# Kernel optimization log

Measured on AMD Instinct MI355X. Metric: run time of the kernel, lower is better.

Reference implementation:

```python
import jax, jax.numpy as jnp
import numpy as np

VOCAB = 32000
HID = 1024
HEADS = 16
HEAD_DIM = HID // HEADS
LAYERS = 8
INTER = 4 * HID
ROPE_BASE = 100000.0
EPS = 1e-5


def setup_inputs() -> dict:
    key = jax.random.key(0)
    ks = jax.random.split(key, 12)
    s = 0.02
    inp = {
        'input_ids': jax.random.randint(ks[0], (2, 2048), 0, VOCAB),
        'embed_W': jax.random.normal(ks[1], (VOCAB, HID), jnp.float32) * s,
        'Wq': jax.random.normal(ks[2], (LAYERS, HID, HID), jnp.float32) * s,
        'Wk': jax.random.normal(ks[3], (LAYERS, HID, HID), jnp.float32) * s,
        'Wv': jax.random.normal(ks[4], (LAYERS, HID, HID), jnp.float32) * s,
        'Wo': jax.random.normal(ks[5], (LAYERS, HID, HID), jnp.float32) * s,
        'Wg': jax.random.normal(ks[6], (LAYERS, HID, INTER), jnp.float32) * s,
        'Wu': jax.random.normal(ks[7], (LAYERS, HID, INTER), jnp.float32) * s,
        'Wd': jax.random.normal(ks[8], (LAYERS, INTER, HID), jnp.float32) * s,
        'norm1_w': jnp.ones((LAYERS, HID), jnp.float32),
        'norm2_w': jnp.ones((LAYERS, HID), jnp.float32),
        'final_norm_w': jnp.ones((HID,), jnp.float32),
        'head_W': jax.random.normal(ks[9], (HID, VOCAB), jnp.float32) * s,
    }
    return inp


def rms_norm(x, w):
    return x * jax.lax.rsqrt(jnp.mean(x * x, axis=-1, keepdims=True) + EPS) * w


def rope_tables(seq_len):
    freq = 1.0 / (ROPE_BASE ** (jnp.arange(0, HEAD_DIM, 2, dtype=jnp.float32) / HEAD_DIM))
    ang = jnp.arange(seq_len, dtype=jnp.float32)[:, None] * freq  # [S, d/2]
    cos = jnp.concatenate([jnp.cos(ang), jnp.cos(ang)], axis=-1)  # [S, d]
    sin = jnp.concatenate([jnp.sin(ang), jnp.sin(ang)], axis=-1)
    return cos, sin


def rotate_half(x):
    h = x.shape[-1] // 2
    return jnp.concatenate([-x[..., h:], x[..., :h]], axis=-1)


def apply_rope(q, k, cos, sin):
    # q,k: [B,S,H,D]; cos,sin: [S,D] -> broadcast over heads via [:,None,:]
    c = cos[:, None, :]
    s = sin[:, None, :]
    return q * c + rotate_half(q) * s, k * c + rotate_half(k) * s


def attention(x, wq, wk, wv, wo, cos, sin, causal_mask):
    B, S, _ = x.shape
    q = (x @ wq).reshape(B, S, HEADS, HEAD_DIM)
    k = (x @ wk).reshape(B, S, HEADS, HEAD_DIM)
    v = (x @ wv).reshape(B, S, HEADS, HEAD_DIM)
    q, k = apply_rope(q, k, cos, sin)
    scores = jnp.einsum('bqhd,bkhd->bhqk', q, k) / np.sqrt(HEAD_DIM)
    scores = jnp.clip(scores, -1000.0, 1000.0)
    scores = jnp.where(causal_mask, jnp.finfo(scores.dtype).min, scores)
    w = jax.nn.softmax(scores.astype(jnp.float32), axis=-1).astype(q.dtype)
    w = jnp.clip(w, 0.0, 1.0)
    ctx = jnp.einsum('bhqk,bkhd->bqhd', w, v).reshape(B, S, HID)
    return ctx @ wo


def reference(input_ids, embed_W, Wq, Wk, Wv, Wo, Wg, Wu, Wd, norm1_w, norm2_w, final_norm_w, head_W):
    B, S = input_ids.shape
    h = embed_W[input_ids]  # [B,S,HID]
    cos, sin = rope_tables(S)
    causal_mask = jnp.triu(jnp.ones((S, S), bool), k=1)[None, None]
    for l in range(LAYERS):
        h = h + attention(rms_norm(h, norm1_w[l]), Wq[l], Wk[l], Wv[l], Wo[l], cos, sin, causal_mask)
        hn = rms_norm(h, norm2_w[l])
        h = h + (jax.nn.silu(hn @ Wg[l]) * (hn @ Wu[l])) @ Wd[l]
    h = rms_norm(h, final_norm_w)
    logits = h @ head_W
    return logits, h
```

## Files before the change

kernel.cpp:

```cpp
#include <hip/hip_runtime.h>

#define T_TOK 4096
#define SEQ   2048
#define HID   1024
#define NH    16
#define HD    64
#define INTER 4096
#define NLAYER 8
#define VOCAB 32000

typedef short short8 __attribute__((ext_vector_type(8)));
typedef float f32x4  __attribute__((ext_vector_type(4)));

__device__ __forceinline__ unsigned short f2bf(float f){
  unsigned int u = __builtin_bit_cast(unsigned int, f);
  u += 0x7fffu + ((u >> 16) & 1u);
  return (unsigned short)(u >> 16);
}
__device__ __forceinline__ float bf2f(unsigned short b){
  unsigned int u = ((unsigned int)b) << 16;
  return __builtin_bit_cast(float, u);
}

#define GLOAD_LDS16(gsrc, ldst) \
  __builtin_amdgcn_global_load_lds((const __attribute__((address_space(1))) void*)(gsrc), \
                                   (__attribute__((address_space(3))) void*)(ldst), 16, 0, 0)

__global__ __launch_bounds__(256) void embed_kernel(const int* __restrict__ ids,
                                                    const float* __restrict__ W,
                                                    float* __restrict__ h){
  int i = blockIdx.x * 256 + threadIdx.x;
  int t = i >> 8, c = i & 255;
  ((float4*)h)[i] = ((const float4*)(W + (size_t)ids[t] * HID))[c];
}

__global__ __launch_bounds__(256) void rope_tab_kernel(float* __restrict__ cosT,
                                                       float* __restrict__ sinT){
  int i = blockIdx.x * 256 + threadIdx.x;
  int s = i >> 5, f = i & 31;
  float inv = expf(-((2.0f * (float)f) / 64.0f) * logf(100000.0f));
  float ang = (float)s * inv;
  cosT[i] = cosf(ang);
  sinT[i] = sinf(ang);
}

__global__ __launch_bounds__(256) void rmsnorm_kernel(const float* __restrict__ h,
                                                      const float* __restrict__ w,
                                                      unsigned short* __restrict__ out,
                                                      float* hcopy){
  int t = blockIdx.x, tid = threadIdx.x;
  float4 v = ((const float4*)(h + (size_t)t * HID))[tid];
  float ss = v.x*v.x + v.y*v.y + v.z*v.z + v.w*v.w;
  #pragma unroll
  for (int m = 1; m < 64; m <<= 1) ss += __shfl_xor(ss, m);
  __shared__ float red[4];
  if ((tid & 63) == 0) red[tid >> 6] = ss;
  __syncthreads();
  float r = rsqrtf((red[0] + red[1] + red[2] + red[3]) * (1.0f / HID) + 1e-5f);
  float4 wv = ((const float4*)w)[tid];
  float nx = v.x * r * wv.x;
  float ny = v.y * r * wv.y;
  float nz = v.z * r * wv.z;
  float nw = v.w * r * wv.w;
  ushort4 o;
  o.x = f2bf(nx); o.y = f2bf(ny); o.z = f2bf(nz); o.w = f2bf(nw);
  ((ushort4*)(out + (size_t)t * HID))[tid] = o;
  if (hcopy){
    float4 hv; hv.x = nx; hv.y = ny; hv.z = nz; hv.w = nw;
    ((float4*)(hcopy + (size_t)t * HID))[tid] = hv;
  }
}

__global__ __launch_bounds__(256) void rope_kernel(unsigned short* __restrict__ q,
                                                   unsigned short* __restrict__ k,
                                                   const float* __restrict__ cosT,
                                                   const float* __restrict__ sinT){
  int i = blockIdx.x * 256 + threadIdx.x;
  int t = i >> 9, rem = i & 511;
  int hh = rem >> 5, f = rem & 31;
  int s = t & (SEQ - 1);
  float c = cosT[s * 32 + f], sn = sinT[s * 32 + f];
  size_t base = (size_t)t * HID + hh * HD + f;
  float q0 = bf2f(q[base]), q1 = bf2f(q[base + 32]);
  q[base]      = f2bf(q0 * c - q1 * sn);
  q[base + 32] = f2bf(q1 * c + q0 * sn);
  float k0 = bf2f(k[base]), k1 = bf2f(k[base + 32]);
  k[base]      = f2bf(k0 * c - k1 * sn);
  k[base + 32] = f2bf(k1 * c + k0 * sn);
}

__global__ __launch_bounds__(256) void convert_w_kernel(const float* __restrict__ W,
                                                        unsigned short* __restrict__ Wt,
                                                        int K, int N){
  __shared__ unsigned short t_lds[64][72];
  W  += (size_t)blockIdx.z * K * N;
  Wt += (size_t)blockIdx.z * K * N;
  const int n0 = blockIdx.x * 64, k0 = blockIdx.y * 64;
  const int tid = threadIdx.x;
  const int tr = tid >> 4, tc = tid & 15;
  #pragma unroll
  for (int i = 0; i < 4; ++i){
    int kk = tr + i * 16;
    float4 v = *(const float4*)(W + (size_t)(k0 + kk) * N + n0 + tc * 4);
    t_lds[tc*4+0][kk] = f2bf(v.x);
    t_lds[tc*4+1][kk] = f2bf(v.y);
    t_lds[tc*4+2][kk] = f2bf(v.z);
    t_lds[tc*4+3][kk] = f2bf(v.w);
  }
  __syncthreads();
  const int n = tid >> 2, cp = tid & 3;
  #pragma unroll
  for (int j = 0; j < 2; ++j){
    int c = cp * 2 + j;
    uint4 d = *(const uint4*)(&t_lds[n][c * 8]);
    *(uint4*)(Wt + (size_t)(n0 + n) * K + k0 + ((c ^ (n & 7)) << 3)) = d;
  }
}

__device__ __forceinline__ void gemm_core(const unsigned short* __restrict__ A,
                                          const unsigned short* __restrict__ Bt,
                                          int K, int m0, int n0,
                                          unsigned short* As, unsigned short* Bs,
                                          f32x4 (&acc)[4][4]){
  const int tid = threadIdx.x;
  const int lane = tid & 63, w = tid >> 6;
  const int l15 = lane & 15, g = lane >> 4;
  const int lr = lane >> 3;
  const int lc = lane & 7;
  const int wr = w >> 1, wc = w & 1;
  const int axor = ((lc ^ lr) << 3);

  #pragma unroll
  for (int m = 0; m < 4; ++m)
    #pragma unroll
    for (int n = 0; n < 4; ++n)
      #pragma unroll
      for (int i = 0; i < 4; ++i) acc[m][n][i] = 0.0f;

  for (int kk = 0; kk < K; kk += 64){
    __syncthreads();
    #pragma unroll
    for (int i = 0; i < 4; ++i){
      int rb = (i * 4 + w) * 8;
      GLOAD_LDS16(A  + (size_t)(m0 + rb + lr) * K + kk + axor,      As + rb * 64);
      GLOAD_LDS16(Bt + (size_t)(n0 + rb + lr) * K + kk + (lc << 3), Bs + rb * 64);
    }
    __syncthreads();
    short8 a[4][2], b[4][2];
    const int x = l15 & 7;
    #pragma unroll
    for (int m = 0; m < 4; ++m){
      int row = wr * 64 + m * 16 + l15;
      a[m][0] = *(const short8*)(As + row * 64 + ((g       ^ x) << 3));
      a[m][1] = *(const short8*)(As + row * 64 + (((4 + g) ^ x) << 3));
    }
    #pragma unroll
    for (int n = 0; n < 4; ++n){
      int row = wc * 64 + n * 16 + l15;
      b[n][0] = *(const short8*)(Bs + row * 64 + ((g       ^ x) << 3));
      b[n][1] = *(const short8*)(Bs + row * 64 + (((4 + g) ^ x) << 3));
    }
    #pragma unroll
    for (int m = 0; m < 4; ++m)
      #pragma unroll
      for (int n = 0; n < 4; ++n){
        acc[m][n] = __builtin_amdgcn_mfma_f32_16x16x32_bf16(a[m][0], b[n][0], acc[m][n], 0, 0, 0);
        acc[m][n] = __builtin_amdgcn_mfma_f32_16x16x32_bf16(a[m][1], b[n][1], acc[m][n], 0, 0, 0);
      }
  }
}

template<int MODE>
__device__ __forceinline__ void gemm_epi(const f32x4 (&acc)[4][4], void* Cout,
                                         const float* __restrict__ resid,
                                         int N, int m0, int n0, int ldt){
  const int tid = threadIdx.x;
  const int lane = tid & 63, w = tid >> 6;
  const int l15 = lane & 15, g = lane >> 4;
  const int wr = w >> 1, wc = w & 1;
  #pragma unroll
  for (int m = 0; m < 4; ++m){
    #pragma unroll
    for (int n = 0; n < 4; ++n){
      int row0 = m0 + wr * 64 + m * 16 + g * 4;
      int col  = n0 + wc * 64 + n * 16 + l15;
      #pragma unroll
      for (int i = 0; i < 4; ++i){
        float v = acc[m][n][i];
        if (MODE == 0){
          ((unsigned short*)Cout)[(size_t)(row0 + i) * N + col] = f2bf(v);
        } else if (MODE == 1){
          size_t idx = (size_t)(row0 + i) * N + col;
          ((float*)Cout)[idx] = resid[idx] + v;
        } else if (MODE == 2){
          ((unsigned short*)Cout)[(size_t)col * ldt + (row0 + i)] = f2bf(v);
        } else {
          ((float*)Cout)[(size_t)(row0 + i) * N + col] = v;
        }
      }
    }
  }
}

template<int MODE>
__global__ __launch_bounds__(256) void gemm_bf16(const unsigned short* __restrict__ A,
                                                 const unsigned short* __restrict__ Bt,
                                                 void* Cout, const float* resid,
                                                 int K, int N, int ldt){
  __shared__ unsigned short As[128 * 64];
  __shared__ unsigned short Bs[128 * 64];
  f32x4 acc[4][4];
  gemm_core(A, Bt, K, blockIdx.x * 128, blockIdx.y * 128, As, Bs, acc);
  gemm_epi<MODE>(acc, Cout, resid, N, blockIdx.x * 128, blockIdx.y * 128, ldt);
}

__global__ __launch_bounds__(256) void gemm_qkv(const unsigned short* __restrict__ A,
                                                const unsigned short* __restrict__ BtQ,
                                                const unsigned short* __restrict__ BtK,
                                                const unsigned short* __restrict__ BtV,
                                                unsigned short* qb, unsigned short* kb,
                                                unsigned short* vt){
  __shared__ unsigned short As[128 * 64];
  __shared__ unsigned short Bs[128 * 64];
  const int nb = blockIdx.y, sel = nb >> 3, n0 = (nb & 7) * 128;
  const unsigned short* Bt = (sel == 0) ? BtQ : (sel == 1) ? BtK : BtV;
  f32x4 acc[4][4];
  gemm_core(A, Bt, HID, blockIdx.x * 128, n0, As, Bs, acc);
  if (sel == 0)      gemm_epi<0>(acc, qb, nullptr, HID, blockIdx.x * 128, n0, 0);
  else if (sel == 1) gemm_epi<0>(acc, kb, nullptr, HID, blockIdx.x * 128, n0, 0);
  else               gemm_epi<2>(acc, vt, nullptr, HID, blockIdx.x * 128, n0, T_TOK);
}

__global__ __launch_bounds__(256) void gemm_gu(const unsigned short* __restrict__ A,
                                               const unsigned short* __restrict__ BtG,
                                               const unsigned short* __restrict__ BtU,
                                               unsigned short* gb, unsigned short* ub){
  __shared__ unsigned short As[128 * 64];
  __shared__ unsigned short Bs[128 * 64];
  const int nb = blockIdx.y, sel = nb >> 5, n0 = (nb & 31) * 128;
  f32x4 acc[4][4];
  gemm_core(A, sel ? BtU : BtG, HID, blockIdx.x * 128, n0, As, Bs, acc);
  gemm_epi<0>(acc, sel ? ub : gb, nullptr, INTER, blockIdx.x * 128, n0, 0);
}

__global__ __launch_bounds__(256, 2) void gemm_f32b(const unsigned short* __restrict__ A,
                                                    const float* __restrict__ Bw,
                                                    float* __restrict__ Cout,
                                                    int M, int N, int K){
  __shared__ unsigned short As[128 * 32];
  __shared__ unsigned short Bs[128 * 32];
  const int tid = threadIdx.x;
  const int lane = tid & 63, wid = tid >> 6;
  const int l15 = lane & 15, g = lane >> 4;
  const int wr = wid >> 1, wc = wid & 1;
  const int m0 = blockIdx.x * 128, n0 = blockIdx.y * 128;
  const int bcol = tid & 127, bhalf = tid >> 7;
  f32x4 acc[4][4];
  #pragma unroll
  for (int m = 0; m < 4; ++m)
    #pragma unroll
    for (int n = 0; n < 4; ++n)
      #pragma unroll
      for (int i = 0; i < 4; ++i) acc[m][n][i] = 0.0f;
  for (int kk = 0; kk < K; kk += 32){
    __syncthreads();
    #pragma unroll
    for (int cc = 0; cc < 2; ++cc){
      int c = tid + cc * 256;
      int row = c >> 2, kc = (c & 3) << 3;
      uint4 d = *(const uint4*)(A + (size_t)(m0 + row) * K + kk + kc);
      *(uint4*)(&As[row * 32 + kc]) = d;
    }
    {
      const float* bp = Bw + (size_t)(kk + bhalf * 16) * N + n0 + bcol;
      float f[16];
      #pragma unroll
      for (int j = 0; j < 16; ++j) f[j] = bp[(size_t)j * N];
      unsigned int pk[8];
      #pragma unroll
      for (int j = 0; j < 8; ++j)
        pk[j] = (unsigned int)f2bf(f[2*j]) | ((unsigned int)f2bf(f[2*j+1]) << 16);
      int sw = (bcol >> 1) & 3;
      int c0 = ((bhalf << 1)     ) ^ sw;
      int c1 = ((bhalf << 1) | 1 ) ^ sw;
      uint4 w0; w0.x = pk[0]; w0.y = pk[1]; w0.z = pk[2]; w0.w = pk[3];
      uint4 w1; w1.x = pk[4]; w1.y = pk[5]; w1.z = pk[6]; w1.w = pk[7];
      *(uint4*)(&Bs[bcol * 32 + c0 * 8]) = w0;
      *(uint4*)(&Bs[bcol * 32 + c1 * 8]) = w1;
    }
    __syncthreads();
    short8 a[4], b[4];
    #pragma unroll
    for (int m = 0; m < 4; ++m)
      a[m] = *(const short8*)(&As[(wr*64 + m*16 + l15) * 32 + g*8]);
    #pragma unroll
    for (int n = 0; n < 4; ++n){
      int col = wc*64 + n*16 + l15;
      b[n] = *(const short8*)(&Bs[col * 32 + (g ^ ((col >> 1) & 3)) * 8]);
    }
    #pragma unroll
    for (int m = 0; m < 4; ++m)
      #pragma unroll
      for (int n = 0; n < 4; ++n)
        acc[m][n] = __builtin_amdgcn_mfma_f32_16x16x32_bf16(a[m], b[n], acc[m][n], 0, 0, 0);
  }
  #pragma unroll
  for (int m = 0; m < 4; ++m)
    #pragma unroll
    for (int n = 0; n < 4; ++n){
      int row0 = m0 + wr*64 + m*16 + g*4;
      int col  = n0 + wc*64 + n*16 + l15;
      #pragma unroll
      for (int i = 0; i < 4; ++i)
        Cout[(size_t)(row0 + i) * N + col] = acc[m][n][i];
    }
}

__global__ __launch_bounds__(256) void attn_kernel(const unsigned short* __restrict__ q,
                                                   const unsigned short* __restrict__ k,
                                                   const unsigned short* __restrict__ vt,
                                                   unsigned short* __restrict__ ctx){
  const int tid = threadIdx.x;
  const int lane = tid & 63, w = tid >> 6;
  const int l15 = lane & 15, g = lane >> 4;
  const int q0 = blockIdx.x * 128 + w * 32;
  const int hh = blockIdx.y;
  const int b  = blockIdx.z;
  const int tb = b * SEQ;

  __shared__ unsigned short Ks[64][72];
  __shared__ unsigned short Vs[64][72];
  __shared__ unsigned short Ps[4][2][16][72];

  short8 qa[2][2];
  #pragma unroll
  for (int qs = 0; qs < 2; ++qs)
    #pragma unroll
    for (int kd = 0; kd < 2; ++kd)
      qa[qs][kd] = *(const short8*)(q + (size_t)(tb + q0 + qs*16 + l15) * HID + hh*HD + kd*32 + g*8);

  float m_run[2][4], l_run[2][4];
  f32x4 o_acc[2][4];
  #pragma unroll
  for (int qs = 0; qs < 2; ++qs)
    #pragma unroll
    for (int i = 0; i < 4; ++i){ m_run[qs][i] = -1e30f; l_run[qs][i] = 0.0f; }
  #pragma unroll
  for (int qs = 0; qs < 2; ++qs)
    #pragma unroll
    for (int dt = 0; dt < 4; ++dt)
      #pragma unroll
      for (int i = 0; i < 4; ++i) o_acc[qs][dt][i] = 0.0f;

  const int ntile = ((blockIdx.x * 128 + 127) >> 6) + 1;
  const int sr = tid >> 2, sc = (tid & 3) * 2;
  for (int kt = 0; kt < ntile; ++kt){
    const int kv0 = kt * 64;
    __syncthreads();
    *(uint4*)(&Ks[sr][sc*8])   = *(const uint4*)(k  + (size_t)(tb+kv0+sr)*HID + hh*HD + sc*8);
    *(uint4*)(&Ks[sr][sc*8+8]) = *(const uint4*)(k  + (size_t)(tb+kv0+sr)*HID + hh*HD + sc*8+8);
    *(uint4*)(&Vs[sr][sc*8])   = *(const uint4*)(vt + (size_t)(hh*HD+sr)*T_TOK + tb + kv0 + sc*8);
    *(uint4*)(&Vs[sr][sc*8+8]) = *(const uint4*)(vt + (size_t)(hh*HD+sr)*T_TOK + tb + kv0 + sc*8+8);
    __syncthreads();

    short8 kf[4][2];
    #pragma unroll
    for (int ct = 0; ct < 4; ++ct)
      #pragma unroll
      for (int kd = 0; kd < 2; ++kd)
        kf[ct][kd] = *(const short8*)(&Ks[ct*16 + l15][kd*32 + g*8]);

    #pragma unroll
    for (int qs = 0; qs < 2; ++qs){
      float pv[4][4];
      #pragma unroll
      for (int ct = 0; ct < 4; ++ct){
        f32x4 scv;
        #pragma unroll
        for (int i = 0; i < 4; ++i) scv[i] = 0.0f;
        scv = __builtin_amdgcn_mfma_f32_16x16x32_bf16(qa[qs][0], kf[ct][0], scv, 0, 0, 0);
        scv = __builtin_amdgcn_mfma_f32_16x16x32_bf16(qa[qs][1], kf[ct][1], scv, 0, 0, 0);
        #pragma unroll
        for (int i = 0; i < 4; ++i){
          float s = scv[i] * 0.125f;
          s = fminf(fmaxf(s, -1000.0f), 1000.0f);
          int row = q0 + qs*16 + g*4 + i;
          int col = kv0 + ct*16 + l15;
          pv[ct][i] = (col > row) ? -1e30f : s;
        }
      }
      #pragma unroll
      for (int i = 0; i < 4; ++i){
        float mx = fmaxf(fmaxf(pv[0][i], pv[1][i]), fmaxf(pv[2][i], pv[3][i]));
        #pragma unroll
        for (int msk = 1; msk < 16; msk <<= 1) mx = fmaxf(mx, __shfl_xor(mx, msk));
        float mnew = fmaxf(m_run[qs][i], mx);
        float scale = __expf(m_run[qs][i] - mnew);
        float psum = 0.0f;
        #pragma unroll
        for (int ct = 0; ct < 4; ++ct){
          float p = __expf(pv[ct][i] - mnew);
          pv[ct][i] = p; psum += p;
        }
        #pragma unroll
        for (int msk = 1; msk < 16; msk <<= 1) psum += __shfl_xor(psum, msk);
        l_run[qs][i] = l_run[qs][i] * scale + psum;
        m_run[qs][i] = mnew;
        #pragma unroll
        for (int dt = 0; dt < 4; ++dt) o_acc[qs][dt][i] *= scale;
      }
      #pragma unroll
      for (int ct = 0; ct < 4; ++ct)
        #pragma unroll
        for (int i = 0; i < 4; ++i)
          Ps[w][qs][g*4 + i][ct*16 + l15] = f2bf(pv[ct][i]);
    }
    #pragma unroll
    for (int ks = 0; ks < 2; ++ks){
      short8 vb[4];
      #pragma unroll
      for (int dt = 0; dt < 4; ++dt)
        vb[dt] = *(const short8*)(&Vs[dt*16 + l15][ks*32 + g*8]);
      #pragma unroll
      for (int qs = 0; qs < 2; ++qs){
        short8 ap = *(const short8*)(&Ps[w][qs][l15][ks*32 + g*8]);
        #pragma unroll
        for (int dt = 0; dt < 4; ++dt)
          o_acc[qs][dt] = __builtin_amdgcn_mfma_f32_16x16x32_bf16(ap, vb[dt], o_acc[qs][dt], 0, 0, 0);
      }
    }
  }
  #pragma unroll
  for (int qs = 0; qs < 2; ++qs)
    #pragma unroll
    for (int dt = 0; dt < 4; ++dt)
      #pragma unroll
      for (int i = 0; i < 4; ++i){
        float o = o_acc[qs][dt][i] / l_run[qs][i];
        ctx[(size_t)(tb + q0 + qs*16 + g*4 + i) * HID + hh*HD + dt*16 + l15] = f2bf(o);
      }
}

__global__ __launch_bounds__(256) void silu_mul_kernel(unsigned short* __restrict__ gbuf,
                                                       const unsigned short* __restrict__ ubuf){
  int i = blockIdx.x * 256 + threadIdx.x;
  ushort4 gv = ((const ushort4*)gbuf)[i];
  ushort4 uv = ((const ushort4*)ubuf)[i];
  ushort4 o;
  float x;
  x = bf2f(gv.x); o.x = f2bf((x / (1.0f + __expf(-x))) * bf2f(uv.x));
  x = bf2f(gv.y); o.y = f2bf((x / (1.0f + __expf(-x))) * bf2f(uv.y));
  x = bf2f(gv.z); o.z = f2bf((x / (1.0f + __expf(-x))) * bf2f(uv.z));
  x = bf2f(gv.w); o.w = f2bf((x / (1.0f + __expf(-x))) * bf2f(uv.w));
  ((ushort4*)gbuf)[i] = o;
}

extern "C" void kernel_launch(void* const* d_in, const int* in_sizes, int n_in,
                              void* d_out, int out_size, void* d_ws, size_t ws_size,
                              hipStream_t stream){
  const int*   ids    = (const int*)d_in[0];
  const float* embedW = (const float*)d_in[1];
  const float* Wq = (const float*)d_in[2];
  const float* Wk = (const float*)d_in[3];
  const float* Wv = (const float*)d_in[4];
  const float* Wo = (const float*)d_in[5];
  const float* Wg = (const float*)d_in[6];
  const float* Wu = (const float*)d_in[7];
  const float* Wd = (const float*)d_in[8];
  const float* n1 = (const float*)d_in[9];
  const float* n2 = (const float*)d_in[10];
  const float* nf = (const float*)d_in[11];
  const float* Wh = (const float*)d_in[12];
  float* out = (float*)d_out;

  char* scb = (char*)d_out;
  unsigned short* qb  = (unsigned short*)(scb + 0);
  unsigned short* kb  = (unsigned short*)(scb + 8388608);
  unsigned short* vtb = (unsigned short*)(scb + 16777216);
  unsigned short* ctx = (unsigned short*)(scb + 25165824);
  unsigned short* gb  = (unsigned short*)(scb + 33554432);
  unsigned short* ub  = (unsigned short*)(scb + 67108864);
  float* cosT = (float*)(scb + 100663296);
  float* sinT = (float*)(scb + 100925440);
  float* h_fallback   = (float*)(scb + 104857600);
  unsigned short* WtQ = (unsigned short*)(scb + 134217728);
  unsigned short* WtK = (unsigned short*)(scb + 150994944);
  unsigned short* WtV = (unsigned short*)(scb + 167772160);
  unsigned short* WtO = (unsigned short*)(scb + 184549376);
  unsigned short* WtG = (unsigned short*)(scb + 201326592);
  unsigned short* WtU = (unsigned short*)(scb + 268435456);
  unsigned short* WtD = (unsigned short*)(scb + 335544320);

  unsigned short* xn = (unsigned short*)d_ws;
  float* h = (ws_size >= 25165824u) ? (float*)((char*)d_ws + 8388608) : h_fallback;
  unsigned short* WhT = (ws_size >= 90701824u)
                      ? (unsigned short*)((char*)d_ws + 25165824) : nullptr;

  convert_w_kernel<<<dim3(16, 16, 8), 256, 0, stream>>>(Wq, WtQ, HID, HID);
  convert_w_kernel<<<dim3(16, 16, 8), 256, 0, stream>>>(Wk, WtK, HID, HID);
  convert_w_kernel<<<dim3(16, 16, 8), 256, 0, stream>>>(Wv, WtV, HID, HID);
  convert_w_kernel<<<dim3(16, 16, 8), 256, 0, stream>>>(Wo, WtO, HID, HID);
  convert_w_kernel<<<dim3(64, 16, 8), 256, 0, stream>>>(Wg, WtG, HID, INTER);
  convert_w_kernel<<<dim3(64, 16, 8), 256, 0, stream>>>(Wu, WtU, HID, INTER);
  convert_w_kernel<<<dim3(16, 64, 8), 256, 0, stream>>>(Wd, WtD, INTER, HID);
  if (WhT)
    convert_w_kernel<<<dim3(500, 16, 1), 256, 0, stream>>>(Wh, WhT, HID, VOCAB);

  embed_kernel<<<4096, 256, 0, stream>>>(ids, embedW, h);
  rope_tab_kernel<<<256, 256, 0, stream>>>(cosT, sinT);

  for (int l = 0; l < NLAYER; ++l){
    rmsnorm_kernel<<<4096, 256, 0, stream>>>(h, n1 + l*HID, xn, nullptr);
    gemm_qkv<<<dim3(32, 24), 256, 0, stream>>>(xn, WtQ + (size_t)l*HID*HID,
                                               WtK + (size_t)l*HID*HID,
                                               WtV + (size_t)l*HID*HID, qb, kb, vtb);
    rope_kernel<<<8192, 256, 0, stream>>>(qb, kb, cosT, sinT);
    attn_kernel<<<dim3(16, 16, 2), 256, 0, stream>>>(qb, kb, vtb, ctx);
    gemm_bf16<1><<<dim3(32, 8), 256, 0, stream>>>(ctx, WtO + (size_t)l*HID*HID,
                                                  h, h, HID, HID, 0);
    rmsnorm_kernel<<<4096, 256, 0, stream>>>(h, n2 + l*HID, xn, nullptr);
    gemm_gu<<<dim3(32, 64), 256, 0, stream>>>(xn, WtG + (size_t)l*HID*INTER,
                                              WtU + (size_t)l*HID*INTER, gb, ub);
    silu_mul_kernel<<<16384, 256, 0, stream>>>(gb, ub);
    gemm_bf16<1><<<dim3(32, 8), 256, 0, stream>>>(gb, WtD + (size_t)l*HID*INTER,
                                                  h, h, INTER, HID, 0);
  }

  rmsnorm_kernel<<<4096, 256, 0, stream>>>(h, nf, xn, out + 131072000);
  if (WhT)
    gemm_bf16<3><<<dim3(32, 250), 256, 0, stream>>>(xn, WhT, out, nullptr, HID, VOCAB, 0);
  else
    gemm_f32b<<<dim3(32, 250), 256, 0, stream>>>(xn, Wh, out, T_TOK, VOCAB, HID);
}
```

Measured before the change: 3.834 ms.

## Rework GEMM K-tiling and flash attention tiling with causal skip and lazy rescale

The GEMM core drops from a 64-wide to a 32-wide K step, removes the XOR swizzle in both the weight transpose and the LDS reads, and halves LDS use per block. The f32 epilogue now uses nontemporal stores. Attention moves to 128-key tiles, launches the heaviest query blocks first, skips fully masked column tiles on the diagonal, and only rescales the running max when it grows by more than 8. This aims for better occupancy and less wasted work on masked tiles, but the unswizzled LDS layout risks bank conflicts and the shorter K step doubles the barriers per GEMM.

```diff
diff --git a/kernel.cpp b/kernel.cpp
--- a/kernel.cpp
+++ b/kernel.cpp
@@ -113,7 +113,7 @@
   for (int j = 0; j < 2; ++j){
     int c = cp * 2 + j;
     uint4 d = *(const uint4*)(&t_lds[n][c * 8]);
-    *(uint4*)(Wt + (size_t)(n0 + n) * K + k0 + ((c ^ (n & 7)) << 3)) = d;
+    *(uint4*)(Wt + (size_t)(n0 + n) * K + k0 + c * 8) = d;
   }
 }
 
@@ -125,10 +125,9 @@
   const int tid = threadIdx.x;
   const int lane = tid & 63, w = tid >> 6;
   const int l15 = lane & 15, g = lane >> 4;
-  const int lr = lane >> 3;
-  const int lc = lane & 7;
   const int wr = w >> 1, wc = w & 1;
-  const int axor = ((lc ^ lr) << 3);
+  const int srow = lane >> 2;
+  const int soff = (lane & 3) << 3;
 
   #pragma unroll
   for (int m = 0; m < 4; ++m)
@@ -137,36 +136,25 @@
       #pragma unroll
       for (int i = 0; i < 4; ++i) acc[m][n][i] = 0.0f;
 
-  for (int kk = 0; kk < K; kk += 64){
+  for (int kk = 0; kk < K; kk += 32){
     __syncthreads();
-    #pragma unroll
-    for (int i = 0; i < 4; ++i){
-      int rb = (i * 4 + w) * 8;
-      GLOAD_LDS16(A  + (size_t)(m0 + rb + lr) * K + kk + axor,      As + rb * 64);
-      GLOAD_LDS16(Bt + (size_t)(n0 + rb + lr) * K + kk + (lc << 3), Bs + rb * 64);
-    }
+    GLOAD_LDS16(A  + (size_t)(m0 +      w*16 + srow) * K + kk + soff, As + (w*16) * 32);
+    GLOAD_LDS16(A  + (size_t)(m0 + 64 + w*16 + srow) * K + kk + soff, As + (64 + w*16) * 32);
+    GLOAD_LDS16(Bt + (size_t)(n0 +      w*16 + srow) * K + kk + soff, Bs + (w*16) * 32);
+    GLOAD_LDS16(Bt + (size_t)(n0 + 64 + w*16 + srow) * K + kk + soff, Bs + (64 + w*16) * 32);
     __syncthreads();
-    short8 a[4][2], b[4][2];
-    const int x = l15 & 7;
-    #pragma unroll
-    for (int m = 0; m < 4; ++m){
-      int row = wr * 64 + m * 16 + l15;
-      a[m][0] = *(const short8*)(As + row * 64 + ((g       ^ x) << 3));
-      a[m][1] = *(const short8*)(As + row * 64 + (((4 + g) ^ x) << 3));
-    }
-    #pragma unroll
-    for (int n = 0; n < 4; ++n){
-      int row = wc * 64 + n * 16 + l15;
-      b[n][0] = *(const short8*)(Bs + row * 64 + ((g       ^ x) << 3));
-      b[n][1] = *(const short8*)(Bs + row * 64 + (((4 + g) ^ x) << 3));
-    }
+    short8 a[4], b[4];
     #pragma unroll
     for (int m = 0; m < 4; ++m)
-      #pragma unroll
-      for (int n = 0; n < 4; ++n){
-        acc[m][n] = __builtin_amdgcn_mfma_f32_16x16x32_bf16(a[m][0], b[n][0], acc[m][n], 0, 0, 0);
-        acc[m][n] = __builtin_amdgcn_mfma_f32_16x16x32_bf16(a[m][1], b[n][1], acc[m][n], 0, 0, 0);
-      }
+      a[m] = *(const short8*)(As + (wr*64 + m*16 + l15) * 32 + g*8);
+    #pragma unroll
+    for (int n = 0; n < 4; ++n)
+      b[n] = *(const short8*)(Bs + (wc*64 + n*16 + l15) * 32 + g*8);
+    #pragma unroll
+    for (int m = 0; m < 4; ++m)
+      #pragma unroll
+      for (int n = 0; n < 4; ++n)
+        acc[m][n] = __builtin_amdgcn_mfma_f32_16x16x32_bf16(a[m], b[n], acc[m][n], 0, 0, 0);
   }
 }
 
@@ -195,7 +183,7 @@
         } else if (MODE == 2){
           ((unsigned short*)Cout)[(size_t)col * ldt + (row0 + i)] = f2bf(v);
         } else {
-          ((float*)Cout)[(size_t)(row0 + i) * N + col] = v;
+          __builtin_nontemporal_store(v, &((float*)Cout)[(size_t)(row0 + i) * N + col]);
         }
       }
     }
@@ -207,8 +195,8 @@
                                                  const unsigned short* __restrict__ Bt,
                                                  void* Cout, const float* resid,
                                                  int K, int N, int ldt){
-  __shared__ unsigned short As[128 * 64];
-  __shared__ unsigned short Bs[128 * 64];
+  __shared__ unsigned short As[128 * 32];
+  __shared__ unsigned short Bs[128 * 32];
   f32x4 acc[4][4];
   gemm_core(A, Bt, K, blockIdx.x * 128, blockIdx.y * 128, As, Bs, acc);
   gemm_epi<MODE>(acc, Cout, resid, N, blockIdx.x * 128, blockIdx.y * 128, ldt);
@@ -220,8 +208,8 @@
                                                 const unsigned short* __restrict__ BtV,
                                                 unsigned short* qb, unsigned short* kb,
                                                 unsigned short* vt){
-  __shared__ unsigned short As[128 * 64];
-  __shared__ unsigned short Bs[128 * 64];
+  __shared__ unsigned short As[128 * 32];
+  __shared__ unsigned short Bs[128 * 32];
   const int nb = blockIdx.y, sel = nb >> 3, n0 = (nb & 7) * 128;
   const unsigned short* Bt = (sel == 0) ? BtQ : (sel == 1) ? BtK : BtV;
   f32x4 acc[4][4];
@@ -235,8 +223,8 @@
                                                const unsigned short* __restrict__ BtG,
                                                const unsigned short* __restrict__ BtU,
                                                unsigned short* gb, unsigned short* ub){
-  __shared__ unsigned short As[128 * 64];
-  __shared__ unsigned short Bs[128 * 64];
+  __shared__ unsigned short As[128 * 32];
+  __shared__ unsigned short Bs[128 * 32];
   const int nb = blockIdx.y, sel = nb >> 5, n0 = (nb & 31) * 128;
   f32x4 acc[4][4];
   gemm_core(A, sel ? BtU : BtG, HID, blockIdx.x * 128, n0, As, Bs, acc);
@@ -323,14 +311,14 @@
   const int tid = threadIdx.x;
   const int lane = tid & 63, w = tid >> 6;
   const int l15 = lane & 15, g = lane >> 4;
-  const int q0 = blockIdx.x * 128 + w * 32;
+  const int bx = (int)gridDim.x - 1 - (int)blockIdx.x;
+  const int q0 = bx * 128 + w * 32;
   const int hh = blockIdx.y;
-  const int b  = blockIdx.z;
-  const int tb = b * SEQ;
-
-  __shared__ unsigned short Ks[64][72];
-  __shared__ unsigned short Vs[64][72];
-  __shared__ unsigned short Ps[4][2][16][72];
+  const int tb = blockIdx.z * SEQ;
+
+  __shared__ unsigned short Ks[128][72];
+  __shared__ unsigned short Vs[64][136];
+  __shared__ unsigned short Ps[4][16][136];
 
   short8 qa[2][2];
   #pragma unroll
@@ -352,81 +340,97 @@
       #pragma unroll
       for (int i = 0; i < 4; ++i) o_acc[qs][dt][i] = 0.0f;
 
-  const int ntile = ((blockIdx.x * 128 + 127) >> 6) + 1;
-  const int sr = tid >> 2, sc = (tid & 3) * 2;
-  for (int kt = 0; kt < ntile; ++kt){
-    const int kv0 = kt * 64;
+  const int krow = tid >> 1, khf = (tid & 1) * 32;
+  const int vrow = tid >> 2, vq  = (tid & 3) * 32;
+
+  for (int kt = 0; kt <= bx; ++kt){
+    const int kv0 = kt * 128;
     __syncthreads();
-    *(uint4*)(&Ks[sr][sc*8])   = *(const uint4*)(k  + (size_t)(tb+kv0+sr)*HID + hh*HD + sc*8);
-    *(uint4*)(&Ks[sr][sc*8+8]) = *(const uint4*)(k  + (size_t)(tb+kv0+sr)*HID + hh*HD + sc*8+8);
-    *(uint4*)(&Vs[sr][sc*8])   = *(const uint4*)(vt + (size_t)(hh*HD+sr)*T_TOK + tb + kv0 + sc*8);
-    *(uint4*)(&Vs[sr][sc*8+8]) = *(const uint4*)(vt + (size_t)(hh*HD+sr)*T_TOK + tb + kv0 + sc*8+8);
+    {
+      const unsigned short* kp = k + (size_t)(tb + kv0 + krow) * HID + hh*HD + khf;
+      #pragma unroll
+      for (int j = 0; j < 4; ++j)
+        *(uint4*)(&Ks[krow][khf + j*8]) = *(const uint4*)(kp + j*8);
+      const unsigned short* vp = vt + (size_t)(hh*HD + vrow) * T_TOK + tb + kv0 + vq;
+      #pragma unroll
+      for (int j = 0; j < 4; ++j)
+        *(uint4*)(&Vs[vrow][vq + j*8]) = *(const uint4*)(vp + j*8);
+    }
     __syncthreads();
-
-    short8 kf[4][2];
-    #pragma unroll
-    for (int ct = 0; ct < 4; ++ct)
-      #pragma unroll
-      for (int kd = 0; kd < 2; ++kd)
-        kf[ct][kd] = *(const short8*)(&Ks[ct*16 + l15][kd*32 + g*8]);
+    const int nct = (kt < bx) ? 8 : (2 * w + 2);
+    const int nks = nct >> 1;
 
     #pragma unroll
     for (int qs = 0; qs < 2; ++qs){
-      float pv[4][4];
-      #pragma unroll
-      for (int ct = 0; ct < 4; ++ct){
-        f32x4 scv;
-        #pragma unroll
-        for (int i = 0; i < 4; ++i) scv[i] = 0.0f;
-        scv = __builtin_amdgcn_mfma_f32_16x16x32_bf16(qa[qs][0], kf[ct][0], scv, 0, 0, 0);
-        scv = __builtin_amdgcn_mfma_f32_16x16x32_bf16(qa[qs][1], kf[ct][1], scv, 0, 0, 0);
-        #pragma unroll
-        for (int i = 0; i < 4; ++i){
-          float s = scv[i] * 0.125f;
-          s = fminf(fmaxf(s, -1000.0f), 1000.0f);
-          int row = q0 + qs*16 + g*4 + i;
-          int col = kv0 + ct*16 + l15;
-          pv[ct][i] = (col > row) ? -1e30f : s;
+      float pv[8][4];
+      #pragma unroll
+      for (int ct = 0; ct < 8; ++ct){
+        if (ct < nct){
+          f32x4 scv;
+          #pragma unroll
+          for (int i = 0; i < 4; ++i) scv[i] = 0.0f;
+          scv = __builtin_amdgcn_mfma_f32_16x16x32_bf16(qa[qs][0],
+                  *(const short8*)(&Ks[ct*16 + l15][g*8]), scv, 0, 0, 0);
+          scv = __builtin_amdgcn_mfma_f32_16x16x32_bf16(qa[qs][1],
+                  *(const short8*)(&Ks[ct*16 + l15][32 + g*8]), scv, 0, 0, 0);
+          #pragma unroll
+          for (int i = 0; i < 4; ++i){
+            float s = scv[i] * 0.125f;
+            s = fminf(fmaxf(s, -1000.0f), 1000.0f);
+            int row = q0 + qs*16 + g*4 + i;
+            int col = kv0 + ct*16 + l15;
+            pv[ct][i] = (col > row) ? -1e30f : s;
+          }
+        } else {
+          #pragma unroll
+          for (int i = 0; i < 4; ++i) pv[ct][i] = -1e30f;
         }
       }
       #pragma unroll
       for (int i = 0; i < 4; ++i){
-        float mx = fmaxf(fmaxf(pv[0][i], pv[1][i]), fmaxf(pv[2][i], pv[3][i]));
+        float mx = pv[0][i];
+        #pragma unroll
+        for (int ct = 1; ct < 8; ++ct) mx = fmaxf(mx, pv[ct][i]);
         #pragma unroll
         for (int msk = 1; msk < 16; msk <<= 1) mx = fmaxf(mx, __shfl_xor(mx, msk));
-        float mnew = fmaxf(m_run[qs][i], mx);
-        float scale = __expf(m_run[qs][i] - mnew);
+        if (!__all(mx <= m_run[qs][i] + 8.0f)){
+          float mnew = fmaxf(m_run[qs][i], mx);
+          float scale = __expf(m_run[qs][i] - mnew);
+          m_run[qs][i] = mnew;
+          l_run[qs][i] *= scale;
+          #pragma unroll
+          for (int dt = 0; dt < 4; ++dt) o_acc[qs][dt][i] *= scale;
+        }
         float psum = 0.0f;
         #pragma unroll
-        for (int ct = 0; ct < 4; ++ct){
-          float p = __expf(pv[ct][i] - mnew);
-          pv[ct][i] = p; psum += p;
+        for (int ct = 0; ct < 8; ++ct){
+          if (ct < nct){
+            float p = __expf(pv[ct][i] - m_run[qs][i]);
+            pv[ct][i] = p; psum += p;
+          } else pv[ct][i] = 0.0f;
         }
         #pragma unroll
         for (int msk = 1; msk < 16; msk <<= 1) psum += __shfl_xor(psum, msk);
-        l_run[qs][i] = l_run[qs][i] * scale + psum;
-        m_run[qs][i] = mnew;
-        #pragma unroll
-        for (int dt = 0; dt < 4; ++dt) o_acc[qs][dt][i] *= scale;
+        l_run[qs][i] += psum;
       }
       #pragma unroll
-      for (int ct = 0; ct < 4; ++ct)
-        #pragma unroll
-        for (int i = 0; i < 4; ++i)
-          Ps[w][qs][g*4 + i][ct*16 + l15] = f2bf(pv[ct][i]);
-    }
-    #pragma unroll
-    for (int ks = 0; ks < 2; ++ks){
-      short8 vb[4];
-      #pragma unroll
-      for (int dt = 0; dt < 4; ++dt)
-        vb[dt] = *(const short8*)(&Vs[dt*16 + l15][ks*32 + g*8]);
-      #pragma unroll
-      for (int qs = 0; qs < 2; ++qs){
-        short8 ap = *(const short8*)(&Ps[w][qs][l15][ks*32 + g*8]);
-        #pragma unroll
-        for (int dt = 0; dt < 4; ++dt)
-          o_acc[qs][dt] = __builtin_amdgcn_mfma_f32_16x16x32_bf16(ap, vb[dt], o_acc[qs][dt], 0, 0, 0);
+      for (int ct = 0; ct < 8; ++ct)
+        if (ct < nct)
+          #pragma unroll
+          for (int i = 0; i < 4; ++i)
+            Ps[w][g*4 + i][ct*16 + l15] = f2bf(pv[ct][i]);
+      #pragma unroll
+      for (int ks = 0; ks < 4; ++ks){
+        if (ks < nks){
+          short8 vb[4];
+          #pragma unroll
+          for (int dt = 0; dt < 4; ++dt)
+            vb[dt] = *(const short8*)(&Vs[dt*16 + l15][ks*32 + g*8]);
+          short8 ap = *(const short8*)(&Ps[w][l15][ks*32 + g*8]);
+          #pragma unroll
+          for (int dt = 0; dt < 4; ++dt)
+            o_acc[qs][dt] = __builtin_amdgcn_mfma_f32_16x16x32_bf16(ap, vb[dt], o_acc[qs][dt], 0, 0, 0);
+        }
       }
     }
   }
```

After: 3.984 ms. +3.9%, slower.
